# Performance work log

Hardware: AMD Instinct MI355X
Metric: run time of the kernel (lower is better)

## Reference

```python
import jax, jax.numpy as jnp
import numpy as np

N_HEAD = 16
D_MODEL = 1024
D_K = 64
D_V = 64
TEMPER = float(np.power(D_MODEL, 0.5))  # NOTE: source scales by sqrt(d_model), not sqrt(d_k)


def setup_inputs() -> dict:
    key = jax.random.key(0)
    ks = jax.random.split(key, 6)
    B, T = 4, 2048
    q = jax.random.normal(ks[0], (B, T, D_MODEL), dtype=jnp.float32)
    k = jax.random.normal(ks[1], (B, T, D_MODEL), dtype=jnp.float32)
    v = jax.random.normal(ks[2], (B, T, D_MODEL), dtype=jnp.float32)
    # xavier_normal for [out, in] = [n_head*d, d_model]; stored as [d_model, n_head*d] for x @ W
    def xavier(kk, fan_out, fan_in):
        std = float(np.sqrt(2.0 / (fan_in + fan_out)))
        return jax.random.normal(kk, (fan_in, fan_out), dtype=jnp.float32) * std
    W_Q = xavier(ks[3], N_HEAD * D_K, D_MODEL)
    W_K = xavier(ks[4], N_HEAD * D_K, D_MODEL)
    W_V = xavier(ks[5], N_HEAD * D_V, D_MODEL)
    return {"q": q, "k": k, "v": v, "W_Q": W_Q, "W_K": W_K, "W_V": W_V}


def reference(q, k, v, W_Q, W_K, W_V):
    B, Tq, _ = q.shape
    Tk = k.shape[1]
    residual = q
    # project and split heads: [B, T, H, d]
    qh = (q @ W_Q).reshape(B, Tq, N_HEAD, D_K)
    kh = (k @ W_K).reshape(B, Tk, N_HEAD, D_K)
    vh = (v @ W_V).reshape(B, Tk, N_HEAD, D_V)
    # scaled dot-product attention (dropout is identity in eval)
    attn = jnp.einsum('bqhd,bkhd->bhqk', qh, kh) / TEMPER
    attn = jax.nn.softmax(attn, axis=-1)
    out = jnp.einsum('bhqk,bkhd->bqhd', attn, vh).reshape(B, Tq, N_HEAD * D_V)
    return out + residual
```

## Files before the change

kernel.cpp:

```cpp
#include <hip/hip_runtime.h>
#include <cstdint>
#include <cstddef>

typedef __bf16 bf16x8 __attribute__((ext_vector_type(8)));
typedef float f32x4 __attribute__((ext_vector_type(4)));
typedef unsigned short u16;
typedef unsigned int u32;

static constexpr int T = 2048;
static constexpr int DM = 1024;
static constexpr float QSCALE = 0.04508422f;

#define GLOBAL_AS __attribute__((address_space(1)))
#define LDS_AS __attribute__((address_space(3)))

__device__ __forceinline__ void gld_lds16(const u16* g, u16* l) {
  __builtin_amdgcn_global_load_lds((const GLOBAL_AS u32*)g, (LDS_AS u32*)l, 16, 0, 0);
}

__device__ __forceinline__ u16 f2bf(float f) {
  u32 u = __builtin_bit_cast(u32, f);
  u += 0x7fffu + ((u >> 16) & 1u);
  return (u16)(u >> 16);
}

__device__ __forceinline__ u32 pkb(float lo, float hi) {
#if __has_builtin(__builtin_amdgcn_cvt_pk_bf16_f32)
  typedef __bf16 bf16x2 __attribute__((ext_vector_type(2)));
  bf16x2 r = __builtin_amdgcn_cvt_pk_bf16_f32(lo, hi);
  return __builtin_bit_cast(u32, r);
#else
  return __builtin_amdgcn_perm(__builtin_bit_cast(u32, hi),
                               __builtin_bit_cast(u32, lo), 0x07060302u);
#endif
}

__device__ __forceinline__ float fexp2(float x) {
#if __has_builtin(__builtin_amdgcn_exp2f)
  return __builtin_amdgcn_exp2f(x);
#else
  return __builtin_exp2f(x);
#endif
}

__global__ __launch_bounds__(256) void xcvt(
    const float* __restrict__ q, const float* __restrict__ k, const float* __restrict__ v,
    u16* __restrict__ oq, u16* __restrict__ ok, u16* __restrict__ ov) {
  const float* X = blockIdx.y == 0 ? q : blockIdx.y == 1 ? k : v;
  u16* O = blockIdx.y == 0 ? oq : blockIdx.y == 1 ? ok : ov;
  const size_t i = ((size_t)blockIdx.x * 256 + threadIdx.x) * 8;
  float4 a0 = *(const float4*)(X + i), a1 = *(const float4*)(X + i + 4);
  uint4 p;
  p.x = pkb(a0.x, a0.y); p.y = pkb(a0.z, a0.w);
  p.z = pkb(a1.x, a1.y); p.w = pkb(a1.z, a1.w);
  *(uint4*)(O + i) = p;
}

__global__ __launch_bounds__(256) void wt_kernel(
    const float* __restrict__ W0, const float* __restrict__ W1, const float* __restrict__ W2,
    u16* __restrict__ O0, u16* __restrict__ O1, u16* __restrict__ O2) {
  const float* W = blockIdx.z == 0 ? W0 : blockIdx.z == 1 ? W1 : W2;
  u16* O = blockIdx.z == 0 ? O0 : blockIdx.z == 1 ? O1 : O2;
  const float sc = blockIdx.z == 0 ? QSCALE : 1.0f;
  const int k0 = blockIdx.x * 64, n0 = blockIdx.y * 64;
  __shared__ float tile[64][68];
  const int tid = threadIdx.x;
#pragma unroll
  for (int it = 0; it < 4; ++it) {
    int chunk = tid + it * 256;
    int r = chunk >> 4, c4 = (chunk & 15) * 4;
    *(float4*)&tile[r][c4] = *(const float4*)(W + (size_t)(k0 + r) * DM + n0 + c4);
  }
  __syncthreads();
#pragma unroll
  for (int it = 0; it < 4; ++it) {
    int chunk = tid + it * 256;
    int n = chunk >> 4, k4 = (chunk & 15) * 4;
    ushort4 o;
    o.x = f2bf(tile[k4 + 0][n] * sc);
    o.y = f2bf(tile[k4 + 1][n] * sc);
    o.z = f2bf(tile[k4 + 2][n] * sc);
    o.w = f2bf(tile[k4 + 3][n] * sc);
    *(ushort4*)(O + (size_t)(n0 + n) * DM + k0 + k4) = o;
  }
}

__global__ __launch_bounds__(256) void gemm_proj(
    const u16* __restrict__ Xq, const u16* __restrict__ Xk, const u16* __restrict__ Xv,
    const u16* __restrict__ Wq, const u16* __restrict__ Wk, const u16* __restrict__ Wv,
    u16* __restrict__ Oq, u16* __restrict__ Ok, u16* __restrict__ Ov) {
  const int z = blockIdx.z;
  const u16* X = z == 0 ? Xq : z == 1 ? Xk : Xv;
  const u16* Wt = z == 0 ? Wq : z == 1 ? Wk : Wv;
  u16* O = z == 0 ? Oq : z == 1 ? Ok : Ov;
  const int m0 = blockIdx.x * 128, n0 = blockIdx.y * 128;
  __shared__ u16 Al[128][32];
  __shared__ u16 Bl[128][32];
  const int tid = threadIdx.x, w = tid >> 6, lane = tid & 63;
  const int c16 = lane & 15, quad = lane >> 4;
  const int wm = (w >> 1) * 64, wn = (w & 1) * 64;
  const int rL = lane >> 2;
  const int cL = ((lane & 3) ^ (rL & 3)) * 8;
  const int sA = (quad ^ (c16 & 3)) * 8;
  f32x4 acc[4][4] = {};
  for (int kk = 0; kk < 1024; kk += 32) {
    __syncthreads();
    {
      const u16* ga = X + (size_t)(m0 + w * 16 + rL) * DM + kk + cL;
      gld_lds16(ga, &Al[w * 16][0]);
      gld_lds16(ga + (size_t)64 * DM, &Al[64 + w * 16][0]);
      const u16* gb = Wt + (size_t)(n0 + w * 16 + rL) * DM + kk + cL;
      gld_lds16(gb, &Bl[w * 16][0]);
      gld_lds16(gb + (size_t)64 * DM, &Bl[64 + w * 16][0]);
    }
    __syncthreads();
    bf16x8 af[4], bfr[4];
#pragma unroll
    for (int t = 0; t < 4; ++t) af[t] = *(const bf16x8*)&Al[wm + t * 16 + c16][sA];
#pragma unroll
    for (int t = 0; t < 4; ++t) bfr[t] = *(const bf16x8*)&Bl[wn + t * 16 + c16][sA];
#pragma unroll
    for (int mt = 0; mt < 4; ++mt)
#pragma unroll
      for (int nt = 0; nt < 4; ++nt)
        acc[mt][nt] = __builtin_amdgcn_mfma_f32_16x16x32_bf16(af[mt], bfr[nt], acc[mt][nt], 0, 0, 0);
  }
#pragma unroll
  for (int mt = 0; mt < 4; ++mt)
#pragma unroll
    for (int nt = 0; nt < 4; ++nt)
#pragma unroll
      for (int r = 0; r < 4; ++r) {
        size_t row = m0 + wm + mt * 16 + quad * 4 + r;
        size_t col = n0 + wn + nt * 16 + c16;
        O[row * DM + col] = f2bf(acc[mt][nt][r]);
      }
}

__global__ __launch_bounds__(256) void vt_kernel(const u16* __restrict__ VH, u16* __restrict__ VHt) {
  const int tt = blockIdx.x & 31, bh = blockIdx.x >> 5;
  const int b = bh >> 4, h = bh & 15;
  __shared__ u16 tile[64][80];
  const int tid = threadIdx.x;
#pragma unroll
  for (int it = 0; it < 2; ++it) {
    int chunk = tid + it * 256;
    int t = chunk >> 3, c8 = (chunk & 7) * 8;
    *(uint4*)&tile[t][c8] = *(const uint4*)(VH + (size_t)(b * T + tt * 64 + t) * DM + h * 64 + c8);
  }
  __syncthreads();
#pragma unroll
  for (int it = 0; it < 2; ++it) {
    int chunk = tid + it * 256;
    int d = chunk >> 3, t8 = (chunk & 7) * 8;
    union { uint4 u; u16 s[8]; } pk;
#pragma unroll
    for (int j = 0; j < 8; ++j) pk.s[j] = tile[t8 + j][d];
    *(uint4*)(VHt + ((size_t)bh * 64 + d) * T + tt * 64 + t8) = pk.u;
  }
}

__global__ __launch_bounds__(256, 2) void flash_kernel(
    const u16* __restrict__ QH, const u16* __restrict__ KH, const u16* __restrict__ VHt,
    const float* __restrict__ res, float* __restrict__ out) {
  const int blk = blockIdx.x;
  const int x = blk & 7, g = blk >> 3;
  const int bh = x * 8 + (g & 7);
  const int qb = g >> 3;
  const int b = bh >> 4, h = bh & 15;
  const int tid = threadIdx.x, w = tid >> 6, lane = tid & 63;
  const int c16 = lane & 15, quad = lane >> 4;
  __shared__ u16 Kl[64][64];
  __shared__ u16 Vt[64][64];
  __shared__ u16 Pl[4][4][16][88];
  __shared__ float Ll[4][4][16];
  const int qbase = qb * 256 + w * 64;
  bf16x8 bq[4][2];
#pragma unroll
  for (int qi = 0; qi < 4; ++qi) {
    const u16* qp = QH + (size_t)(b * T + qbase + qi * 16 + c16) * DM + h * 64 + quad * 8;
    bq[qi][0] = *(const bf16x8*)qp;
    bq[qi][1] = *(const bf16x8*)(qp + 32);
  }
  f32x4 acc[4][4] = {};
  float rs[4] = {0.f, 0.f, 0.f, 0.f};
  const int rk = lane >> 3;
  const int ck8 = ((lane & 7) ^ rk) * 8;
  const u16* kg = KH + (size_t)(b * T) * DM + h * 64 + ck8;
  const u16* vg = VHt + ((size_t)bh * 64 + w * 16 + rk) * T + ck8;
  const int swzq = c16 & 7;
  for (int kt = 0; kt < 32; ++kt) {
    __syncthreads();
    {
      const u16* kg0 = kg + (size_t)(kt * 64 + w * 16 + rk) * DM;
      gld_lds16(kg0, &Kl[w * 16][0]);
      gld_lds16(kg0 + (size_t)8 * DM, &Kl[w * 16 + 8][0]);
      const u16* vg0 = vg + kt * 64;
      gld_lds16(vg0, &Vt[w * 16][0]);
      gld_lds16(vg0 + (size_t)8 * T, &Vt[w * 16 + 8][0]);
    }
    __syncthreads();
    bf16x8 ak[4][2];
#pragma unroll
    for (int mt = 0; mt < 4; ++mt) {
      const int r = mt * 16 + c16;
      ak[mt][0] = *(const bf16x8*)&Kl[r][(quad ^ swzq) * 8];
      ak[mt][1] = *(const bf16x8*)&Kl[r][((quad + 4) ^ swzq) * 8];
    }
#pragma unroll
    for (int qi = 0; qi < 4; ++qi) {
#pragma unroll
      for (int mt = 0; mt < 4; ++mt) {
        f32x4 st = {};
        st = __builtin_amdgcn_mfma_f32_16x16x32_bf16(ak[mt][0], bq[qi][0], st, 0, 0, 0);
        st = __builtin_amdgcn_mfma_f32_16x16x32_bf16(ak[mt][1], bq[qi][1], st, 0, 0, 0);
        const float p0 = fexp2(st[0]), p1 = fexp2(st[1]);
        const float p2 = fexp2(st[2]), p3 = fexp2(st[3]);
        rs[qi] += (p0 + p1) + (p2 + p3);
        uint2 pw;
        pw.x = pkb(p0, p1);
        pw.y = pkb(p2, p3);
        *(uint2*)&Pl[w][qi][c16][mt * 16 + quad * 4] = pw;
      }
    }
    bf16x8 bv[4][2];
#pragma unroll
    for (int nt = 0; nt < 4; ++nt) {
      const int r = nt * 16 + c16;
      bv[nt][0] = *(const bf16x8*)&Vt[r][(quad ^ swzq) * 8];
      bv[nt][1] = *(const bf16x8*)&Vt[r][((quad + 4) ^ swzq) * 8];
    }
    asm volatile("s_waitcnt lgkmcnt(0)" ::: "memory");
#pragma unroll
    for (int qi = 0; qi < 4; ++qi) {
      const bf16x8 ap0 = *(const bf16x8*)&Pl[w][qi][c16][quad * 8];
      const bf16x8 ap1 = *(const bf16x8*)&Pl[w][qi][c16][32 + quad * 8];
#pragma unroll
      for (int nt = 0; nt < 4; ++nt) {
        acc[qi][nt] = __builtin_amdgcn_mfma_f32_16x16x32_bf16(ap0, bv[nt][0], acc[qi][nt], 0, 0, 0);
        acc[qi][nt] = __builtin_amdgcn_mfma_f32_16x16x32_bf16(ap1, bv[nt][1], acc[qi][nt], 0, 0, 0);
      }
    }
  }
#pragma unroll
  for (int qi = 0; qi < 4; ++qi) {
    float t = rs[qi];
    t += __shfl_xor(t, 16, 64);
    t += __shfl_xor(t, 32, 64);
    if (quad == 0) Ll[w][qi][c16] = t;
  }
  asm volatile("s_waitcnt lgkmcnt(0)" ::: "memory");
#pragma unroll
  for (int qi = 0; qi < 4; ++qi) {
    const f32x4 lv = *(const f32x4*)&Ll[w][qi][quad * 4];
#pragma unroll
    for (int r = 0; r < 4; ++r) {
      const float inv = 1.0f / lv[r];
      const size_t rowbase = (size_t)(b * T + qbase + qi * 16 + quad * 4 + r) * DM + h * 64;
#pragma unroll
      for (int nt = 0; nt < 4; ++nt) {
        const size_t idx = rowbase + nt * 16 + c16;
        out[idx] = acc[qi][nt][r] * inv + res[idx];
      }
    }
  }
}

extern "C" void kernel_launch(void* const* d_in, const int* in_sizes, int n_in,
                              void* d_out, int out_size, void* d_ws, size_t ws_size,
                              hipStream_t stream) {
  const float* q = (const float*)d_in[0];
  const float* k = (const float*)d_in[1];
  const float* v = (const float*)d_in[2];
  const float* WQ = (const float*)d_in[3];
  const float* WK = (const float*)d_in[4];
  const float* WV = (const float*)d_in[5];
  char* ws = (char*)d_ws;
  const size_t PH = (size_t)8192 * 1024 * 2;
  const size_t WT = (size_t)1024 * 1024 * 2;
  u16* XqB = (u16*)d_out;
  u16* XkB = (u16*)d_out + (size_t)8192 * 1024;
  u16* XvB = (u16*)(ws);
  u16* WtQ = (u16*)(ws + PH);
  u16* WtK = (u16*)(ws + PH + WT);
  u16* WtV = (u16*)(ws + PH + 2 * WT);
  u16* QH  = (u16*)(ws + PH + 3 * WT);
  u16* KH  = (u16*)(ws + 2 * PH + 3 * WT);
  u16* VH  = (u16*)(ws + 3 * PH + 3 * WT);
  u16* VHt = XvB;

  xcvt<<<dim3(4096, 3), 256, 0, stream>>>(q, k, v, XqB, XkB, XvB);
  wt_kernel<<<dim3(16, 16, 3), 256, 0, stream>>>(WQ, WK, WV, WtQ, WtK, WtV);
  gemm_proj<<<dim3(64, 8, 3), 256, 0, stream>>>(XqB, XkB, XvB, WtQ, WtK, WtV, QH, KH, VH);
  vt_kernel<<<2048, 256, 0, stream>>>(VH, VHt);
  flash_kernel<<<512, 256, 0, stream>>>(QH, KH, VHt, q, (float*)d_out);
}
```

Baseline: 301.1 us.

## Fuse V transpose into projection GEMM, deepen K tile, swizzle P buffer

The V projection GEMM now writes its output directly in transposed per-head layout, so the separate vt_kernel launch and its round trip through memory go away. The projection GEMM takes 64-wide K slices per barrier with an XOR-swizzled LDS layout and remaps blocks for XCD locality. The flash kernel's P scratch buffer drops its padding in favour of an XOR swizzle, and the PV loop is reordered to reuse the P fragments. Both kernels ask for 3 blocks per CU, which constrains register use and risks spilling; the transposed stores from the GEMM are narrower, 8-byte writes.

```diff
diff --git a/kernel.cpp b/kernel.cpp
--- a/kernel.cpp
+++ b/kernel.cpp
@@ -85,82 +85,81 @@
   }
 }
 
-__global__ __launch_bounds__(256) void gemm_proj(
+__global__ __launch_bounds__(256, 3) void gemm_proj(
     const u16* __restrict__ Xq, const u16* __restrict__ Xk, const u16* __restrict__ Xv,
     const u16* __restrict__ Wq, const u16* __restrict__ Wk, const u16* __restrict__ Wv,
-    u16* __restrict__ Oq, u16* __restrict__ Ok, u16* __restrict__ Ov) {
-  const int z = blockIdx.z;
+    u16* __restrict__ Oq, u16* __restrict__ Ok, u16* __restrict__ VHt) {
+  const int z = blockIdx.y;
   const u16* X = z == 0 ? Xq : z == 1 ? Xk : Xv;
   const u16* Wt = z == 0 ? Wq : z == 1 ? Wk : Wv;
-  u16* O = z == 0 ? Oq : z == 1 ? Ok : Ov;
-  const int m0 = blockIdx.x * 128, n0 = blockIdx.y * 128;
-  __shared__ u16 Al[128][32];
-  __shared__ u16 Bl[128][32];
+  const int xcd = blockIdx.x & 7, j = blockIdx.x >> 3;
+  const int n0 = (j & 7) * 128;
+  const int m0 = (xcd * 8 + (j >> 3)) * 128;
+  __shared__ u16 Al[128][64];
+  __shared__ u16 Bl[128][64];
   const int tid = threadIdx.x, w = tid >> 6, lane = tid & 63;
   const int c16 = lane & 15, quad = lane >> 4;
   const int wm = (w >> 1) * 64, wn = (w & 1) * 64;
-  const int rL = lane >> 2;
-  const int cL = ((lane & 3) ^ (rL & 3)) * 8;
-  const int sA = (quad ^ (c16 & 3)) * 8;
+  const int rk = lane >> 3;
+  const int ck = ((lane & 7) ^ rk) * 8;
+  const int swz = c16 & 7;
   f32x4 acc[4][4] = {};
-  for (int kk = 0; kk < 1024; kk += 32) {
-    __syncthreads();
-    {
-      const u16* ga = X + (size_t)(m0 + w * 16 + rL) * DM + kk + cL;
-      gld_lds16(ga, &Al[w * 16][0]);
-      gld_lds16(ga + (size_t)64 * DM, &Al[64 + w * 16][0]);
-      const u16* gb = Wt + (size_t)(n0 + w * 16 + rL) * DM + kk + cL;
-      gld_lds16(gb, &Bl[w * 16][0]);
-      gld_lds16(gb + (size_t)64 * DM, &Bl[64 + w * 16][0]);
-    }
-    __syncthreads();
-    bf16x8 af[4], bfr[4];
-#pragma unroll
-    for (int t = 0; t < 4; ++t) af[t] = *(const bf16x8*)&Al[wm + t * 16 + c16][sA];
-#pragma unroll
-    for (int t = 0; t < 4; ++t) bfr[t] = *(const bf16x8*)&Bl[wn + t * 16 + c16][sA];
+  const u16* ga = X + (size_t)(m0 + w * 32 + rk) * DM + ck;
+  const u16* gb = Wt + (size_t)(n0 + w * 32 + rk) * DM + ck;
+  for (int kk = 0; kk < 1024; kk += 64) {
+    __syncthreads();
+#pragma unroll
+    for (int i = 0; i < 4; ++i) {
+      gld_lds16(ga + kk + (size_t)(i * 8) * DM, &Al[w * 32 + i * 8][0]);
+      gld_lds16(gb + kk + (size_t)(i * 8) * DM, &Bl[w * 32 + i * 8][0]);
+    }
+    __syncthreads();
+#pragma unroll
+    for (int s = 0; s < 2; ++s) {
+      bf16x8 af[4], bfr[4];
+#pragma unroll
+      for (int t = 0; t < 4; ++t) af[t] = *(const bf16x8*)&Al[wm + t * 16 + c16][((quad + 4 * s) ^ swz) * 8];
+#pragma unroll
+      for (int t = 0; t < 4; ++t) bfr[t] = *(const bf16x8*)&Bl[wn + t * 16 + c16][((quad + 4 * s) ^ swz) * 8];
+#pragma unroll
+      for (int mt = 0; mt < 4; ++mt)
+#pragma unroll
+        for (int nt = 0; nt < 4; ++nt)
+          acc[mt][nt] = __builtin_amdgcn_mfma_f32_16x16x32_bf16(af[mt], bfr[nt], acc[mt][nt], 0, 0, 0);
+    }
+  }
+  if (z < 2) {
+    u16* O = z == 0 ? Oq : Ok;
 #pragma unroll
     for (int mt = 0; mt < 4; ++mt)
 #pragma unroll
       for (int nt = 0; nt < 4; ++nt)
-        acc[mt][nt] = __builtin_amdgcn_mfma_f32_16x16x32_bf16(af[mt], bfr[nt], acc[mt][nt], 0, 0, 0);
-  }
-#pragma unroll
-  for (int mt = 0; mt < 4; ++mt)
-#pragma unroll
-    for (int nt = 0; nt < 4; ++nt)
-#pragma unroll
-      for (int r = 0; r < 4; ++r) {
-        size_t row = m0 + wm + mt * 16 + quad * 4 + r;
-        size_t col = n0 + wn + nt * 16 + c16;
-        O[row * DM + col] = f2bf(acc[mt][nt][r]);
-      }
-}
-
-__global__ __launch_bounds__(256) void vt_kernel(const u16* __restrict__ VH, u16* __restrict__ VHt) {
-  const int tt = blockIdx.x & 31, bh = blockIdx.x >> 5;
-  const int b = bh >> 4, h = bh & 15;
-  __shared__ u16 tile[64][80];
-  const int tid = threadIdx.x;
-#pragma unroll
-  for (int it = 0; it < 2; ++it) {
-    int chunk = tid + it * 256;
-    int t = chunk >> 3, c8 = (chunk & 7) * 8;
-    *(uint4*)&tile[t][c8] = *(const uint4*)(VH + (size_t)(b * T + tt * 64 + t) * DM + h * 64 + c8);
-  }
-  __syncthreads();
-#pragma unroll
-  for (int it = 0; it < 2; ++it) {
-    int chunk = tid + it * 256;
-    int d = chunk >> 3, t8 = (chunk & 7) * 8;
-    union { uint4 u; u16 s[8]; } pk;
-#pragma unroll
-    for (int j = 0; j < 8; ++j) pk.s[j] = tile[t8 + j][d];
-    *(uint4*)(VHt + ((size_t)bh * 64 + d) * T + tt * 64 + t8) = pk.u;
-  }
-}
-
-__global__ __launch_bounds__(256, 2) void flash_kernel(
+#pragma unroll
+        for (int r = 0; r < 4; ++r) {
+          size_t row = m0 + wm + mt * 16 + quad * 4 + r;
+          size_t col = n0 + wn + nt * 16 + c16;
+          O[row * DM + col] = f2bf(acc[mt][nt][r]);
+        }
+  } else {
+#pragma unroll
+    for (int mt = 0; mt < 4; ++mt)
+#pragma unroll
+      for (int nt = 0; nt < 4; ++nt) {
+        const int row0 = m0 + wm + mt * 16 + quad * 4;
+        const int col = n0 + wn + nt * 16 + c16;
+        const int bb = row0 >> 11, t0 = row0 & 2047;
+        const int hh = col >> 6, dd = col & 63;
+        ushort4 o;
+        o.x = f2bf(acc[mt][nt][0]);
+        o.y = f2bf(acc[mt][nt][1]);
+        o.z = f2bf(acc[mt][nt][2]);
+        o.w = f2bf(acc[mt][nt][3]);
+        *(ushort4*)(VHt + ((size_t)((bb * 16 + hh) * 64 + dd)) * T + t0) = o;
+      }
+  }
+}
+
+__global__ __launch_bounds__(256, 3) void flash_kernel(
     const u16* __restrict__ QH, const u16* __restrict__ KH, const u16* __restrict__ VHt,
     const float* __restrict__ res, float* __restrict__ out) {
   const int blk = blockIdx.x;
@@ -170,9 +169,10 @@
   const int b = bh >> 4, h = bh & 15;
   const int tid = threadIdx.x, w = tid >> 6, lane = tid & 63;
   const int c16 = lane & 15, quad = lane >> 4;
+  const int swzq = c16 & 7;
   __shared__ u16 Kl[64][64];
   __shared__ u16 Vt[64][64];
-  __shared__ u16 Pl[4][4][16][88];
+  __shared__ u16 Pl[4][4][16][64];
   __shared__ float Ll[4][4][16];
   const int qbase = qb * 256 + w * 64;
   bf16x8 bq[4][2];
@@ -188,7 +188,6 @@
   const int ck8 = ((lane & 7) ^ rk) * 8;
   const u16* kg = KH + (size_t)(b * T) * DM + h * 64 + ck8;
   const u16* vg = VHt + ((size_t)bh * 64 + w * 16 + rk) * T + ck8;
-  const int swzq = c16 & 7;
   for (int kt = 0; kt < 32; ++kt) {
     __syncthreads();
     {
@@ -200,45 +199,48 @@
       gld_lds16(vg0 + (size_t)8 * T, &Vt[w * 16 + 8][0]);
     }
     __syncthreads();
-    bf16x8 ak[4][2];
-#pragma unroll
-    for (int mt = 0; mt < 4; ++mt) {
-      const int r = mt * 16 + c16;
-      ak[mt][0] = *(const bf16x8*)&Kl[r][(quad ^ swzq) * 8];
-      ak[mt][1] = *(const bf16x8*)&Kl[r][((quad + 4) ^ swzq) * 8];
-    }
+    {
+      bf16x8 ak[4][2];
+#pragma unroll
+      for (int mt = 0; mt < 4; ++mt) {
+        const int r = mt * 16 + c16;
+        ak[mt][0] = *(const bf16x8*)&Kl[r][(quad ^ swzq) * 8];
+        ak[mt][1] = *(const bf16x8*)&Kl[r][((4 + quad) ^ swzq) * 8];
+      }
+#pragma unroll
+      for (int qi = 0; qi < 4; ++qi) {
+#pragma unroll
+        for (int mt = 0; mt < 4; ++mt) {
+          f32x4 st = {};
+          st = __builtin_amdgcn_mfma_f32_16x16x32_bf16(ak[mt][0], bq[qi][0], st, 0, 0, 0);
+          st = __builtin_amdgcn_mfma_f32_16x16x32_bf16(ak[mt][1], bq[qi][1], st, 0, 0, 0);
+          const float p0 = fexp2(st[0]), p1 = fexp2(st[1]);
+          const float p2 = fexp2(st[2]), p3 = fexp2(st[3]);
+          rs[qi] += (p0 + p1) + (p2 + p3);
+          uint2 pw;
+          pw.x = pkb(p0, p1);
+          pw.y = pkb(p2, p3);
+          const int col = (((mt * 2 + (quad >> 1)) ^ swzq) * 8) + (quad & 1) * 4;
+          *(uint2*)&Pl[w][qi][c16][col] = pw;
+        }
+      }
+    }
+    asm volatile("s_waitcnt lgkmcnt(0)" ::: "memory");
+    bf16x8 ap[4][2];
 #pragma unroll
     for (int qi = 0; qi < 4; ++qi) {
-#pragma unroll
-      for (int mt = 0; mt < 4; ++mt) {
-        f32x4 st = {};
-        st = __builtin_amdgcn_mfma_f32_16x16x32_bf16(ak[mt][0], bq[qi][0], st, 0, 0, 0);
-        st = __builtin_amdgcn_mfma_f32_16x16x32_bf16(ak[mt][1], bq[qi][1], st, 0, 0, 0);
-        const float p0 = fexp2(st[0]), p1 = fexp2(st[1]);
-        const float p2 = fexp2(st[2]), p3 = fexp2(st[3]);
-        rs[qi] += (p0 + p1) + (p2 + p3);
-        uint2 pw;
-        pw.x = pkb(p0, p1);
-        pw.y = pkb(p2, p3);
-        *(uint2*)&Pl[w][qi][c16][mt * 16 + quad * 4] = pw;
-      }
-    }
-    bf16x8 bv[4][2];
+      ap[qi][0] = *(const bf16x8*)&Pl[w][qi][c16][(quad ^ swzq) * 8];
+      ap[qi][1] = *(const bf16x8*)&Pl[w][qi][c16][((4 + quad) ^ swzq) * 8];
+    }
 #pragma unroll
     for (int nt = 0; nt < 4; ++nt) {
       const int r = nt * 16 + c16;
-      bv[nt][0] = *(const bf16x8*)&Vt[r][(quad ^ swzq) * 8];
-      bv[nt][1] = *(const bf16x8*)&Vt[r][((quad + 4) ^ swzq) * 8];
-    }
-    asm volatile("s_waitcnt lgkmcnt(0)" ::: "memory");
-#pragma unroll
-    for (int qi = 0; qi < 4; ++qi) {
-      const bf16x8 ap0 = *(const bf16x8*)&Pl[w][qi][c16][quad * 8];
-      const bf16x8 ap1 = *(const bf16x8*)&Pl[w][qi][c16][32 + quad * 8];
-#pragma unroll
-      for (int nt = 0; nt < 4; ++nt) {
-        acc[qi][nt] = __builtin_amdgcn_mfma_f32_16x16x32_bf16(ap0, bv[nt][0], acc[qi][nt], 0, 0, 0);
-        acc[qi][nt] = __builtin_amdgcn_mfma_f32_16x16x32_bf16(ap1, bv[nt][1], acc[qi][nt], 0, 0, 0);
+      const bf16x8 bv0 = *(const bf16x8*)&Vt[r][(quad ^ swzq) * 8];
+      const bf16x8 bv1 = *(const bf16x8*)&Vt[r][((4 + quad) ^ swzq) * 8];
+#pragma unroll
+      for (int qi = 0; qi < 4; ++qi) {
+        acc[qi][nt] = __builtin_amdgcn_mfma_f32_16x16x32_bf16(ap[qi][0], bv0, acc[qi][nt], 0, 0, 0);
+        acc[qi][nt] = __builtin_amdgcn_mfma_f32_16x16x32_bf16(ap[qi][1], bv1, acc[qi][nt], 0, 0, 0);
       }
     }
   }
@@ -286,12 +288,10 @@
   u16* WtV = (u16*)(ws + PH + 2 * WT);
   u16* QH  = (u16*)(ws + PH + 3 * WT);
   u16* KH  = (u16*)(ws + 2 * PH + 3 * WT);
-  u16* VH  = (u16*)(ws + 3 * PH + 3 * WT);
-  u16* VHt = XvB;
+  u16* VHt = (u16*)(ws + 3 * PH + 3 * WT);
 
   xcvt<<<dim3(4096, 3), 256, 0, stream>>>(q, k, v, XqB, XkB, XvB);
   wt_kernel<<<dim3(16, 16, 3), 256, 0, stream>>>(WQ, WK, WV, WtQ, WtK, WtV);
-  gemm_proj<<<dim3(64, 8, 3), 256, 0, stream>>>(XqB, XkB, XvB, WtQ, WtK, WtV, QH, KH, VH);
-  vt_kernel<<<2048, 256, 0, stream>>>(VH, VHt);
+  gemm_proj<<<dim3(512, 3), 256, 0, stream>>>(XqB, XkB, XvB, WtQ, WtK, WtV, QH, KH, VHt);
   flash_kernel<<<512, 256, 0, stream>>>(QH, KH, VHt, q, (float*)d_out);
 }
```

New measurement: 349.4 us. 1.16x slower.
